# Kernel optimization log

Hardware: AMD Instinct MI355X
Metric: run time of the kernel (lower is better)

## Reference

```python
import jax, jax.numpy as jnp
from jax import lax
import numpy as np

# Model constants (from init_kwargs)
N = 256      # encoder channels
K = 16       # encoder kernel
S = 8        # encoder stride
BOT = 256    # bottleneck dim
NM = 8       # number of BiMamba blocks
DS = 16      # d_state
DC = 4       # d_conv
DI = 512     # d_inner = expand * bot_dim
DTR = 16     # dt_rank = ceil(bot_dim/16)
BATCH = 2
T = 8000


def silu(x):
    return x * jax.nn.sigmoid(x)


def rmsnorm(x, w, eps=1e-5):
    return x * w / jnp.sqrt(jnp.mean(x * x, axis=-1, keepdims=True) + eps)


def selective_scan(xc, dt, Bm, Cm, A, Dp):
    # xc, dt: [B,L,DI]; Bm, Cm: [B,L,DS]; A: [DI,DS]; Dp: [DI]
    Bsz = xc.shape[0]

    def step(h, inp):
        dt_t, B_t, C_t, x_t = inp          # [B,DI],[B,DS],[B,DS],[B,DI]
        dA = jnp.exp(dt_t[:, :, None] * A)  # [B,DI,DS]
        h = dA * h + (dt_t * x_t)[:, :, None] * B_t[:, None, :]
        y = jnp.einsum('bds,bs->bd', h, C_t)
        return h, y

    h0 = jnp.zeros((Bsz, DI, DS), xc.dtype)
    xs = (jnp.swapaxes(dt, 0, 1), jnp.swapaxes(Bm, 0, 1),
          jnp.swapaxes(Cm, 0, 1), jnp.swapaxes(xc, 0, 1))
    _, ys = lax.scan(step, h0, xs)
    return jnp.swapaxes(ys, 0, 1) + xc * Dp


def mamba_dir(x, inw, cw, cb, xpw, dtw, dtb, Alog, Dp, ow):
    # x: [B,L,BOT] -> [B,L,BOT], one Mamba direction
    xz = x @ inw.T                              # [B,L,2*DI]
    xi, z = jnp.split(xz, 2, axis=-1)
    # causal depthwise conv over time
    xc = lax.conv_general_dilated(jnp.swapaxes(xi, 1, 2), cw[:, None, :], (1,),
                                  [(DC - 1, 0)], feature_group_count=DI,
                                  dimension_numbers=('NCH', 'OIH', 'NCH'))
    xc = jnp.swapaxes(silu(xc + cb[None, :, None]), 1, 2)   # [B,L,DI]
    xdbl = xc @ xpw.T                          # [B,L,DTR+2*DS]
    dt = jax.nn.softplus(xdbl[..., :DTR] @ dtw.T + dtb)     # [B,L,DI]
    Bm = xdbl[..., DTR:DTR + DS]
    Cm = xdbl[..., DTR + DS:]
    A = -jnp.exp(Alog)                          # [DI,DS]
    y = selective_scan(xc, dt, Bm, Cm, A, Dp)
    return (y * silu(z)) @ ow.T


def _forward(mixture, enc_w, dec_w, gn_w, gn_b, bot_w, bot_b, blk_norm_w,
             in_w, conv_w, conv_b, xproj_w, dt_w, dt_b, A_log, Dmat, out_w,
             normf_w, mask_w, mask_b):
    # Encoder: Conv1d(1,N,K,stride=S) + ReLU -> mixture_w [B,N,L]
    mw = lax.conv_general_dilated(mixture[:, None, :], enc_w, (S,), 'VALID',
                                  dimension_numbers=('NCH', 'OIH', 'NCH'))
    mw = jax.nn.relu(mw)
    # GroupNorm(1, N): normalize over (C,L) per sample
    mu = jnp.mean(mw, axis=(1, 2), keepdims=True)
    var = jnp.var(mw, axis=(1, 2), keepdims=True)
    x = (mw - mu) / jnp.sqrt(var + 1e-5) * gn_w[None, :, None] + gn_b[None, :, None]
    # 1x1 bottleneck conv -> [B,L,BOT]
    x = jnp.einsum('on,bnl->bol', bot_w, x) + bot_b[None, :, None]
    x = jnp.swapaxes(x, 1, 2)
    # BiMamba blocks: pre-RMSNorm, fwd + reversed Mamba, residual
    for i in range(NM):
        xn = rmsnorm(x, blk_norm_w[i])
        yf = mamba_dir(xn, in_w[i, 0], conv_w[i, 0], conv_b[i, 0], xproj_w[i, 0],
                       dt_w[i, 0], dt_b[i, 0], A_log[i, 0], Dmat[i, 0], out_w[i, 0])
        yb = jnp.flip(mamba_dir(jnp.flip(xn, 1), in_w[i, 1], conv_w[i, 1],
                                conv_b[i, 1], xproj_w[i, 1], dt_w[i, 1],
                                dt_b[i, 1], A_log[i, 1], Dmat[i, 1], out_w[i, 1]), 1)
        x = x + yf + yb
    x = rmsnorm(x, normf_w)
    x = jnp.swapaxes(x, 1, 2)                  # [B,BOT,L]
    # mask head: 1x1 conv -> [B, C*N=N, L], ReLU mask (C=1)
    masks = jnp.einsum('ob,bbl->obl'.replace('bbl', 'xbl').replace('obl', 'xol'), mask_w, x)  # placeholder
    masks = jnp.einsum('ob,xbl->xol', mask_w, x) + mask_b[None, :, None]
    masks = jax.nn.relu(masks)
    masked = mw * masks                        # [B,N,L]
    # Decoder: ConvTranspose1d(N,1,K,stride=S,bias=False)
    wt = jnp.swapaxes(jnp.flip(dec_w, -1), 0, 1)   # [1,N,K]
    y = lax.conv_general_dilated(masked, wt, (1,), [(K - 1, K - 1)],
                                 lhs_dilation=(S,),
                                 dimension_numbers=('NCH', 'OIH', 'NCH'))
    return y[:, 0, :]                          # [B,T], C=1 squeezed


def setup_inputs() -> dict:
    key = jax.random.key(0)
    ks = jax.random.split(key, 12)

    def nrm(k, shape, s=0.05):
        return jax.random.normal(k, shape, jnp.float32) * s

    inp = {
        'mixture': jax.random.normal(ks[0], (BATCH, T), jnp.float32),
        'enc_w': nrm(ks[1], (N, 1, K), 0.1),
        'dec_w': nrm(ks[2], (N, 1, K), 0.1),
        'gn_w': jnp.ones((N,), jnp.float32),
        'gn_b': jnp.zeros((N,), jnp.float32),
        'bot_w': nrm(ks[3], (BOT, N)),
        'bot_b': jnp.zeros((BOT,), jnp.float32),
        'blk_norm_w': jnp.ones((NM, BOT), jnp.float32),
        'in_w': nrm(ks[4], (NM, 2, 2 * DI, BOT)),
        'conv_w': nrm(ks[5], (NM, 2, DI, DC), 0.2),
        'conv_b': jnp.zeros((NM, 2, DI), jnp.float32),
        'xproj_w': nrm(ks[6], (NM, 2, DTR + 2 * DS, DI)),
        'dt_w': nrm(ks[7], (NM, 2, DI, DTR), 0.1),
        'dt_b': jnp.full((NM, 2, DI), -4.0, jnp.float32),
        'A_log': jnp.log(jnp.arange(1., DS + 1, dtype=jnp.float32)) * jnp.ones((NM, 2, DI, DS), jnp.float32),
        'Dmat': jnp.ones((NM, 2, DI), jnp.float32),
        'out_w': nrm(ks[8], (NM, 2, BOT, DI)),
        'normf_w': jnp.ones((BOT,), jnp.float32),
        'mask_w': nrm(ks[9], (N, BOT)),
        'mask_b': jnp.zeros((N,), jnp.float32),
    }
    return inp


def reference(mixture, enc_w, dec_w, gn_w, gn_b, bot_w, bot_b, blk_norm_w,
              in_w, conv_w, conv_b, xproj_w, dt_w, dt_b, A_log, Dmat, out_w,
              normf_w, mask_w, mask_b):
    return _forward(mixture, enc_w, dec_w, gn_w, gn_b, bot_w, bot_b,
                    blk_norm_w, in_w, conv_w, conv_b, xproj_w, dt_w, dt_b,
                    A_log, Dmat, out_w, normf_w, mask_w, mask_b)
```

## Files before the change

kernel.cpp:

```cpp
#include <hip/hip_runtime.h>
#include <cstdint>
#include <cmath>

#define LQ   999
#define BLQ  1998
#define NCH  256
#define NLTOT 255744
#define NCHK 16
#define CHL  64

typedef __attribute__((ext_vector_type(8))) short bf16x8;
typedef __attribute__((ext_vector_type(4))) float f32x4;

__device__ inline ushort f2bf(float f) {
  uint32_t u = __float_as_uint(f);
  u += 0x7fff + ((u >> 16) & 1);
  return (ushort)(u >> 16);
}

__global__ __launch_bounds__(256) void k_quant(const float* __restrict__ inw,
                                               const float* __restrict__ outw,
                                               const float* __restrict__ dtw,
                                               ushort* __restrict__ inwh,
                                               ushort* __restrict__ outwh,
                                               float* __restrict__ dtwt) {
  int i = blockIdx.x * 256 + threadIdx.x;
  if (i < 4194304) inwh[i] = f2bf(inw[i]);
  if (i < 2097152) outwh[i] = f2bf(outw[i]);
  if (i < 131072) {
    int w = i >> 13, d = (i >> 4) & 511, q = i & 15;
    dtwt[(w << 13) + q * 512 + d] = dtw[i];
  }
}

__global__ __launch_bounds__(256) void k_enc(const float* __restrict__ mix,
                                             const float* __restrict__ ew,
                                             float* __restrict__ mw,
                                             float* __restrict__ stats) {
  int t = threadIdx.x;
  int b = blockIdx.x >= LQ;
  int rem = (blockIdx.x - b * LQ) * 256 + t;
  int n = rem / LQ;
  int l = rem - n * LQ;
  const float* mp = mix + b * 8000 + l * 8;
  const float* wp = ew + n * 16;
  float acc = 0.f;
#pragma unroll
  for (int k = 0; k < 16; ++k) acc += mp[k] * wp[k];
  float v = fmaxf(acc, 0.f);
  mw[(b * NCH + n) * LQ + l] = v;
  float s1 = v, s2 = v * v;
#pragma unroll
  for (int off = 32; off >= 1; off >>= 1) {
    s1 += __shfl_xor(s1, off, 64);
    s2 += __shfl_xor(s2, off, 64);
  }
  __shared__ float r1[4], r2[4];
  int wv = t >> 6, lane = t & 63;
  if (lane == 0) { r1[wv] = s1; r2[wv] = s2; }
  __syncthreads();
  if (t == 0) {
    atomicAdd(&stats[b * 2 + 0], r1[0] + r1[1] + r1[2] + r1[3]);
    atomicAdd(&stats[b * 2 + 1], r2[0] + r2[1] + r2[2] + r2[3]);
  }
}

__global__ void k_stats(float* stats) {
  int t = threadIdx.x;
  if (t < 2) {
    float s = stats[t * 2 + 0], q = stats[t * 2 + 1];
    float mu = s / (float)NLTOT;
    float var = q / (float)NLTOT - mu * mu;
    stats[4 + t * 2 + 0] = mu;
    stats[4 + t * 2 + 1] = 1.f / sqrtf(var + 1e-5f);
  }
}

__global__ __launch_bounds__(256) void k_prep(const float* __restrict__ bw,
                                              const float* __restrict__ gw,
                                              const float* __restrict__ gb,
                                              const float* __restrict__ bb,
                                              const float* __restrict__ stats,
                                              float* __restrict__ w2,
                                              float* __restrict__ cc) {
  int o = blockIdx.x, n = threadIdx.x;
  float bwv = bw[o * 256 + n];
  float w2v = bwv * gw[n];
  w2[o * 256 + n] = w2v;
  float s1 = bwv * gb[n], s2 = w2v;
#pragma unroll
  for (int off = 32; off >= 1; off >>= 1) {
    s1 += __shfl_xor(s1, off, 64);
    s2 += __shfl_xor(s2, off, 64);
  }
  __shared__ float r1[4], r2[4];
  int wv = n >> 6, lane = n & 63;
  if (lane == 0) { r1[wv] = s1; r2[wv] = s2; }
  __syncthreads();
  if (n == 0) {
    float a1 = r1[0] + r1[1] + r1[2] + r1[3];
    float a2 = r2[0] + r2[1] + r2[2] + r2[3];
    for (int b = 0; b < 2; ++b)
      cc[b * 256 + o] = bb[o] + a1 - stats[4 + b * 2] * stats[5 + b * 2] * a2;
  }
}

template <bool BF>
__global__ __launch_bounds__(256) void k_rms(const float* __restrict__ x,
                                             const float* __restrict__ w,
                                             float* __restrict__ out,
                                             ushort* __restrict__ outh) {
  int t = threadIdx.x;
  int row = blockIdx.x * 4 + (t >> 6);
  int lane = t & 63;
  if (row >= BLQ) return;
  float4 v = *(const float4*)&x[row * 256 + lane * 4];
  float ss = v.x * v.x + v.y * v.y + v.z * v.z + v.w * v.w;
#pragma unroll
  for (int off = 32; off >= 1; off >>= 1) ss += __shfl_xor(ss, off, 64);
  float r = 1.f / sqrtf(ss * (1.f / 256.f) + 1e-5f);
  float4 wv = *(const float4*)&w[lane * 4];
  float4 o;
  o.x = v.x * wv.x * r; o.y = v.y * wv.y * r;
  o.z = v.z * wv.z * r; o.w = v.w * wv.w * r;
  if (BF) {
    ushort4 oh = {f2bf(o.x), f2bf(o.y), f2bf(o.z), f2bf(o.w)};
    *(ushort4*)&outh[row * 256 + lane * 4] = oh;
  } else {
    *(float4*)&out[row * 256 + lane * 4] = o;
  }
}

template <int MODE>
__global__ __launch_bounds__(256) void gemm64(const float* __restrict__ A,
                                              const float* __restrict__ Bw,
                                              float* __restrict__ C,
                                              const float* __restrict__ aux1,
                                              const float* __restrict__ aux2,
                                              int M, int K,
                                              int aDS, int bDS, int cDS) {
  if (MODE == 4) {
    A += (size_t)blockIdx.z * aDS;
    Bw += (size_t)blockIdx.z * bDS;
    C += (size_t)blockIdx.z * cDS;
  }
  __shared__ float As[16][68];
  __shared__ float Bs[16][68];
  int t = threadIdx.x;
  int m0 = blockIdx.x * 64, n0 = blockIdx.y * 64;
  int tx = t & 15, ty = t >> 4;
  float acc[4][4] = {};
  for (int kk = 0; kk < K; kk += 16) {
    if (MODE == 0) {
#pragma unroll
      for (int j = 0; j < 4; ++j) {
        int e = t + 256 * j;
        int m_ = e & 63, k_ = e >> 6;
        int m = m0 + m_;
        float v = 0.f;
        if (m < M) {
          int bb = m >= LQ;
          int l = m - bb * LQ;
          v = A[(size_t)((bb << 8) + kk + k_) * LQ + l];
        }
        As[k_][m_] = v;
      }
    } else {
      int m_ = t >> 2, k4 = (t & 3) * 4;
      int m = m0 + m_;
      float4 v = make_float4(0.f, 0.f, 0.f, 0.f);
      if (m < M) v = *(const float4*)&A[(size_t)m * K + kk + k4];
      As[k4 + 0][m_] = v.x; As[k4 + 1][m_] = v.y;
      As[k4 + 2][m_] = v.z; As[k4 + 3][m_] = v.w;
    }
    {
      int n_ = t >> 2, k4 = (t & 3) * 4;
      int n = n0 + n_;
      float4 v = make_float4(0.f, 0.f, 0.f, 0.f);
      if (MODE != 4 || n_ < 48)
        v = *(const float4*)&Bw[(size_t)n * K + kk + k4];
      Bs[k4 + 0][n_] = v.x; Bs[k4 + 1][n_] = v.y;
      Bs[k4 + 2][n_] = v.z; Bs[k4 + 3][n_] = v.w;
    }
    __syncthreads();
#pragma unroll
    for (int k = 0; k < 16; ++k) {
      float4 av = *(const float4*)&As[k][ty * 4];
      float4 bv = *(const float4*)&Bs[k][tx * 4];
      acc[0][0] += av.x * bv.x; acc[0][1] += av.x * bv.y; acc[0][2] += av.x * bv.z; acc[0][3] += av.x * bv.w;
      acc[1][0] += av.y * bv.x; acc[1][1] += av.y * bv.y; acc[1][2] += av.y * bv.z; acc[1][3] += av.y * bv.w;
      acc[2][0] += av.z * bv.x; acc[2][1] += av.z * bv.y; acc[2][2] += av.z * bv.z; acc[2][3] += av.z * bv.w;
      acc[3][0] += av.w * bv.x; acc[3][1] += av.w * bv.y; acc[3][2] += av.w * bv.z; acc[3][3] += av.w * bv.w;
    }
    __syncthreads();
  }
#pragma unroll
  for (int i = 0; i < 4; ++i) {
    int m = m0 + ty * 4 + i;
    if (m < M) {
      int n = n0 + tx * 4;
      if (MODE == 0) {
        int bb = m >= LQ;
        float invb = aux1[5 + bb * 2];
        float4 cv = *(const float4*)&aux2[(bb << 8) + n];
        float4 o;
        o.x = acc[i][0] * invb + cv.x; o.y = acc[i][1] * invb + cv.y;
        o.z = acc[i][2] * invb + cv.z; o.w = acc[i][3] * invb + cv.w;
        *(float4*)&C[(size_t)m * 256 + n] = o;
      } else if (MODE == 3) {
        int bb = m >= LQ;
        int l = m - bb * LQ;
        float4 o;
#pragma unroll
        for (int j = 0; j < 4; ++j) {
          int nc = n + j;
          float v = fmaxf(acc[i][j] + aux1[nc], 0.f);
          float mwv = aux2[(size_t)((bb << 8) + nc) * LQ + l];
          ((float*)&o)[j] = v * mwv;
        }
        *(float4*)&C[(size_t)m * 256 + n] = o;
      } else {
#pragma unroll
        for (int j = 0; j < 4; ++j) {
          int nc = n + j;
          if (nc < 48) C[(size_t)m * 48 + nc] = acc[i][j];
        }
      }
    }
  }
}

__global__ __launch_bounds__(256) void k_mm1(const ushort* __restrict__ Ah,
                                             const ushort* __restrict__ Bh,
                                             float* __restrict__ C) {
  int lane = threadIdx.x & 63, wid = threadIdx.x >> 6;
  int mbase = blockIdx.x * 128 + (wid >> 1) * 64;
  int nbase = blockIdx.y * 128 + (wid & 1) * 64;
  int lm = lane & 15, lk = (lane >> 4) * 8;
  f32x4 acc[4][4] = {};
  for (int ks = 0; ks < 256; ks += 32) {
    bf16x8 a[4], b[4];
#pragma unroll
    for (int mi = 0; mi < 4; ++mi) {
      int row = mbase + mi * 16 + lm;
      row = row < BLQ ? row : BLQ - 1;
      a[mi] = *(const bf16x8*)&Ah[(size_t)row * 256 + ks + lk];
    }
#pragma unroll
    for (int ni = 0; ni < 4; ++ni) {
      int nr = nbase + ni * 16 + lm;
      b[ni] = *(const bf16x8*)&Bh[(size_t)nr * 256 + ks + lk];
    }
#pragma unroll
    for (int mi = 0; mi < 4; ++mi)
#pragma unroll
      for (int ni = 0; ni < 4; ++ni)
        acc[mi][ni] = __builtin_amdgcn_mfma_f32_16x16x32_bf16(a[mi], b[ni], acc[mi][ni], 0, 0, 0);
  }
  int rbase = (lane >> 4) * 4;
#pragma unroll
  for (int mi = 0; mi < 4; ++mi)
#pragma unroll
    for (int r = 0; r < 4; ++r) {
      int m = mbase + mi * 16 + rbase + r;
      if (m < BLQ) {
#pragma unroll
        for (int ni = 0; ni < 4; ++ni)
          C[(size_t)m * 2048 + nbase + ni * 16 + lm] = acc[mi][ni][r];
      }
    }
}

__global__ __launch_bounds__(256) void k_mm2(const ushort* __restrict__ Ah,
                                             const ushort* __restrict__ Bh,
                                             float* __restrict__ C) {
  int lane = threadIdx.x & 63, wid = threadIdx.x >> 6;
  int mbase = blockIdx.x * 128 + (wid >> 1) * 64;
  int nbase = blockIdx.y * 128 + (wid & 1) * 64;
  int lm = lane & 15, lk = (lane >> 4) * 8;
  f32x4 acc[4][4] = {};
  for (int ks = 0; ks < 1024; ks += 32) {
    int dir = ks >> 9;
    int di = (ks & 511) + lk;
    const ushort* Ab = Ah + (size_t)dir * BLQ * 512 + di;
    const ushort* Bb = Bh + (size_t)dir * 131072 + di;
    bf16x8 a[4], b[4];
#pragma unroll
    for (int mi = 0; mi < 4; ++mi) {
      int row = mbase + mi * 16 + lm;
      row = row < BLQ ? row : BLQ - 1;
      a[mi] = *(const bf16x8*)&Ab[(size_t)row * 512];
    }
#pragma unroll
    for (int ni = 0; ni < 4; ++ni) {
      int nr = nbase + ni * 16 + lm;
      b[ni] = *(const bf16x8*)&Bb[(size_t)nr * 512];
    }
#pragma unroll
    for (int mi = 0; mi < 4; ++mi)
#pragma unroll
      for (int ni = 0; ni < 4; ++ni)
        acc[mi][ni] = __builtin_amdgcn_mfma_f32_16x16x32_bf16(a[mi], b[ni], acc[mi][ni], 0, 0, 0);
  }
  int rbase = (lane >> 4) * 4;
#pragma unroll
  for (int mi = 0; mi < 4; ++mi)
#pragma unroll
    for (int r = 0; r < 4; ++r) {
      int m = mbase + mi * 16 + rbase + r;
      if (m < BLQ) {
#pragma unroll
        for (int ni = 0; ni < 4; ++ni) {
          size_t idx = (size_t)m * 256 + nbase + ni * 16 + lm;
          C[idx] += acc[mi][ni][r];
        }
      }
    }
}

__global__ __launch_bounds__(256) void k_conv(const float* __restrict__ xz,
                                              const float* __restrict__ cwAll,
                                              const float* __restrict__ cbAll,
                                              float* __restrict__ xc, int blk) {
  int dir = blockIdx.y;
  int flat = blockIdx.x * 256 + threadIdx.x;
  int d = flat & 511, bl = flat >> 9;
  int bb = bl >= LQ;
  int l = bl - bb * LQ;
  int w = blk * 2 + dir;
  const float* cw = cwAll + (size_t)(w * 512 + d) * 4;
  float acc = cbAll[w * 512 + d];
  int zoff = dir * 1024 + d;
#pragma unroll
  for (int j = 0; j < 4; ++j) {
    int ls = (dir == 0) ? (l - 3 + j) : (l + 3 - j);
    if (ls >= 0 && ls < LQ) acc += xz[(size_t)(bb * LQ + ls) * 2048 + zoff] * cw[j];
  }
  float sg = acc / (1.f + __expf(-acc));
  xc[(size_t)(dir * BLQ + bl) * 512 + d] = sg;
}

__global__ __launch_bounds__(256) void k_dt(const float* __restrict__ xdbl,
                                            const float* __restrict__ dtwt,
                                            const float* __restrict__ dtbAll,
                                            float* __restrict__ dtg, int blk) {
  int dir = blockIdx.y;
  int flat = blockIdx.x * 256 + threadIdx.x;
  int d = flat & 511, bl = flat >> 9;
  int w = blk * 2 + dir;
  const float* xd = xdbl + (size_t)(dir * BLQ + bl) * 48;
  const float* Wp = dtwt + (w << 13);
  float acc = dtbAll[w * 512 + d];
#pragma unroll
  for (int q = 0; q < 16; ++q) acc += xd[q] * Wp[q * 512 + d];
  float sp = fmaxf(acc, 0.f) + log1pf(expf(-fabsf(acc)));
  dtg[(size_t)(dir * BLQ + bl) * 512 + d] = sp;
}

__global__ __launch_bounds__(256) void k_scanA(const float* __restrict__ dtg,
                                               const float* __restrict__ xc,
                                               const float* __restrict__ xdbl,
                                               const float* __restrict__ alog,
                                               float* __restrict__ prod,
                                               float* __restrict__ loc, int blk) {
  __shared__ float s_dx[64 * 17 * 2];
  __shared__ float s_bc[64 * 16 * 2];
  int t = threadIdx.x;
  int bid = blockIdx.x;
  int cpair = bid & 7;
  int wb = bid >> 3;
  int dg = wb & 31;
  int b = (wb >> 5) & 1;
  int dir = wb >> 6;
  int dloc = t >> 4, s = t & 15;
  int d0 = dg * 16;
  int d = d0 + dloc;
  int w = blk * 2 + dir;
  int b999 = b * LQ;
  float a2 = -__expf(alog[(size_t)(w * 512 + d) * 16 + s]) * 1.44269504f;
  const float* dtp = dtg + (size_t)dir * BLQ * 512;
  const float* xcp = xc + (size_t)dir * BLQ * 512;
  const float* xdp = xdbl + (size_t)dir * BLQ * 48;
  size_t wbase = (size_t)wb * 4096;
  int c0 = cpair * 2;

  auto stage = [&](int cc) {
    int j16 = t >> 4, dl = t & 15;
#pragma unroll
    for (int it = 0; it < 4; ++it) {
      int j = it * 16 + j16;
      int tg = cc * 64 + j;
      float dtv = 0.f, xv = 0.f;
      if (tg < LQ) {
        int l = dir ? (LQ - 1 - tg) : tg;
        size_t bl = (size_t)(b999 + l);
        dtv = dtp[bl * 512 + d0 + dl];
        xv = xcp[bl * 512 + d0 + dl];
      }
      s_dx[(j * 17 + dl) * 2] = dtv;
      s_dx[(j * 17 + dl) * 2 + 1] = xv;
    }
    int j8 = t >> 5, idx = t & 31;
#pragma unroll
    for (int it = 0; it < 8; ++it) {
      int j = it * 8 + j8;
      int tg = cc * 64 + j;
      float v = 0.f;
      if (tg < LQ) {
        int l = dir ? (LQ - 1 - tg) : tg;
        v = xdp[(size_t)(b999 + l) * 48 + 16 + idx];
      }
      int ss = idx & 15, isC = idx >> 4;
      s_bc[(j * 16 + ss) * 2 + isC] = v;
    }
  };

#pragma unroll
  for (int ci = 0; ci < 2; ++ci) {
    int cc = c0 + ci;
    stage(cc);
    __syncthreads();
    float h = 0.f, pr = 1.f;
#pragma unroll 16
    for (int j = 0; j < 64; ++j) {
      float2 dx = *(float2*)&s_dx[(j * 17 + dloc) * 2];
      float Bv = s_bc[(j * 16 + s) * 2];
      float dA = exp2f(dx.x * a2);
      pr *= dA;
      h = dA * h + dx.x * dx.y * Bv;
    }
    prod[wbase + cc * 256 + t] = pr;
    loc[wbase + cc * 256 + t] = h;
    __syncthreads();
  }
}

__global__ __launch_bounds__(256) void k_scanC(const float* __restrict__ dtg,
                                               const float* __restrict__ xc,
                                               const float* __restrict__ xdbl,
                                               const float* __restrict__ xz,
                                               const float* __restrict__ alog,
                                               const float* __restrict__ dmat,
                                               const float* __restrict__ prod,
                                               const float* __restrict__ loc,
                                               ushort* __restrict__ gh, int blk) {
  __shared__ float s_dx[64 * 17 * 2];
  __shared__ float s_bc[64 * 16 * 2];
  int t = threadIdx.x;
  int bid = blockIdx.x;
  int cpair = bid & 7;
  int wb = bid >> 3;
  int dg = wb & 31;
  int b = (wb >> 5) & 1;
  int dir = wb >> 6;
  int dloc = t >> 4, s = t & 15;
  int d0 = dg * 16;
  int d = d0 + dloc;
  int w = blk * 2 + dir;
  int b999 = b * LQ;
  float a2 = -__expf(alog[(size_t)(w * 512 + d) * 16 + s]) * 1.44269504f;
  float Dd = dmat[w * 512 + d];
  const float* dtp = dtg + (size_t)dir * BLQ * 512;
  const float* xcp = xc + (size_t)dir * BLQ * 512;
  const float* xdp = xdbl + (size_t)dir * BLQ * 48;
  const float* zp = xz + dir * 1024 + 512 + d;
  ushort* gp = gh + (size_t)dir * BLQ * 512;
  size_t wbase = (size_t)wb * 4096;
  int c0 = cpair * 2;

  auto stage = [&](int cc) {
    int j16 = t >> 4, dl = t & 15;
#pragma unroll
    for (int it = 0; it < 4; ++it) {
      int j = it * 16 + j16;
      int tg = cc * 64 + j;
      float dtv = 0.f, xv = 0.f;
      if (tg < LQ) {
        int l = dir ? (LQ - 1 - tg) : tg;
        size_t bl = (size_t)(b999 + l);
        dtv = dtp[bl * 512 + d0 + dl];
        xv = xcp[bl * 512 + d0 + dl];
      }
      s_dx[(j * 17 + dl) * 2] = dtv;
      s_dx[(j * 17 + dl) * 2 + 1] = xv;
    }
    int j8 = t >> 5, idx = t & 31;
#pragma unroll
    for (int it = 0; it < 8; ++it) {
      int j = it * 8 + j8;
      int tg = cc * 64 + j;
      float v = 0.f;
      if (tg < LQ) {
        int l = dir ? (LQ - 1 - tg) : tg;
        v = xdp[(size_t)(b999 + l) * 48 + 16 + idx];
      }
      int ss = idx & 15, isC = idx >> 4;
      s_bc[(j * 16 + ss) * 2 + isC] = v;
    }
  };

  float hs0 = 0.f, hs1 = 0.f;
  {
    float h = 0.f;
#pragma unroll
    for (int ccc = 0; ccc < NCHK; ++ccc) {
      if (ccc == c0) hs0 = h;
      if (ccc == c0 + 1) hs1 = h;
      float prv = prod[wbase + ccc * 256 + t];
      float lov = loc[wbase + ccc * 256 + t];
      h = prv * h + lov;
    }
  }

  auto zload = [&](int cc, int j0n) -> float {
    int tg = cc * 64 + j0n + s;
    if (j0n < 64 && tg < LQ) {
      int l = dir ? (LQ - 1 - tg) : tg;
      return zp[(size_t)(b999 + l) * 2048];
    }
    return 0.f;
  };

#pragma unroll
  for (int ci = 0; ci < 2; ++ci) {
    int cc = c0 + ci;
    stage(cc);
    __syncthreads();
    float h = ci ? hs1 : hs0;
    float keepP = 0.f;
    float zq = zload(cc, 0);
    for (int j0 = 0; j0 < 64; j0 += 16) {
#pragma unroll
      for (int jj = 0; jj < 16; ++jj) {
        int j = j0 + jj;
        float2 dx = *(float2*)&s_dx[(j * 17 + dloc) * 2];
        float2 bc = *(float2*)&s_bc[(j * 16 + s) * 2];
        float dA = exp2f(dx.x * a2);
        h = dA * h + dx.x * dx.y * bc.x;
        float p = h * bc.y;
        p += __shfl_xor(p, 1, 16);
        p += __shfl_xor(p, 2, 16);
        p += __shfl_xor(p, 4, 16);
        p += __shfl_xor(p, 8, 16);
        if (jj == s) keepP = p;
      }
      int tg = cc * 64 + j0 + s;
      float xv = s_dx[((j0 + s) * 17 + dloc) * 2 + 1];
      float zv = zq;
      zq = zload(cc, j0 + 16);
      float sig = 1.f / (1.f + __expf(-zv));
      float y = (keepP + xv * Dd) * (zv * sig);
      if (tg < LQ) {
        int l = dir ? (LQ - 1 - tg) : tg;
        gp[(size_t)(b999 + l) * 512 + d] = f2bf(y);
      }
    }
    __syncthreads();
  }
}

__global__ __launch_bounds__(256) void k_zg(const float* __restrict__ Mt,
                                            const float* __restrict__ dw,
                                            float* __restrict__ Z) {
  __shared__ float sm[16][260];
  __shared__ float sw[256][16];
  int t = threadIdx.x;
  int b = blockIdx.x >= 63;
  int r0 = (blockIdx.x - b * 63) * 16;
#pragma unroll
  for (int it = 0; it < 16; ++it) {
    int e = it * 256 + t;
    int r = e >> 8, c = e & 255;
    int l = r0 + r;
    sm[r][c] = (l < LQ) ? Mt[(size_t)(b * LQ + l) * 256 + c] : 0.f;
    sw[e >> 4][e & 15] = dw[e];
  }
  __syncthreads();
  int lrow = t >> 4, j = t & 15;
  float acc = 0.f;
#pragma unroll 8
  for (int n = 0; n < 256; ++n) acc += sm[lrow][n] * sw[n][j];
  int l = r0 + lrow;
  Z[(size_t)(b * 1008 + l) * 16 + j] = acc;
}

__global__ __launch_bounds__(256) void k_comb(const float* __restrict__ Z,
                                              float* __restrict__ out) {
  int idx = blockIdx.x * 256 + threadIdx.x;
  if (idx >= 16000) return;
  int b = idx >= 8000;
  int tt = idx - b * 8000;
  int l0 = tt >> 3, j0 = tt & 7;
  float v = 0.f;
  if (l0 <= LQ - 1) v += Z[(size_t)(b * 1008 + l0) * 16 + j0];
  if (l0 >= 1) v += Z[(size_t)(b * 1008 + l0 - 1) * 16 + j0 + 8];
  out[idx] = v;
}

extern "C" void kernel_launch(void* const* d_in, const int* in_sizes, int n_in,
                              void* d_out, int out_size, void* d_ws, size_t ws_size,
                              hipStream_t stream) {
  const float* mixture = (const float*)d_in[0];
  const float* enc_w = (const float*)d_in[1];
  const float* dec_w = (const float*)d_in[2];
  const float* gn_w = (const float*)d_in[3];
  const float* gn_b = (const float*)d_in[4];
  const float* bot_w = (const float*)d_in[5];
  const float* bot_b = (const float*)d_in[6];
  const float* blk_norm_w = (const float*)d_in[7];
  const float* in_w = (const float*)d_in[8];
  const float* conv_w = (const float*)d_in[9];
  const float* conv_b = (const float*)d_in[10];
  const float* xproj_w = (const float*)d_in[11];
  const float* dt_w = (const float*)d_in[12];
  const float* dt_b = (const float*)d_in[13];
  const float* A_log = (const float*)d_in[14];
  const float* Dmat = (const float*)d_in[15];
  const float* out_w = (const float*)d_in[16];
  const float* normf_w = (const float*)d_in[17];
  const float* mask_w = (const float*)d_in[18];
  const float* mask_b = (const float*)d_in[19];
  float* outp = (float*)d_out;

  float* W = (float*)d_ws;
  size_t off = 0;
  auto alloc = [&](size_t n) {
    float* p = W + off;
    off += (n + 255) & ~(size_t)255;
    return p;
  };
  float* stats = alloc(8);
  float* w2 = alloc(65536);
  float* cc = alloc(512);
  float* mw = alloc(511488);
  float* x = alloc(511488);
  float* xn = alloc(511488);
  float* xzb = alloc(4091904);
  float* xcb = alloc(2045952);
  float* xdblb = alloc(191808);
  float* dtgb = alloc(2045952);
  float* maskedb = alloc(511488);
  float* prodb = alloc(524288);
  float* locb = alloc(524288);
  float* zbuf = alloc(32256);
  float* dtwt = alloc(131072);
  ushort* xnh = (ushort*)alloc(255744);
  ushort* ghb = (ushort*)alloc(1022976);
  ushort* inwh = (ushort*)alloc(2097152);
  ushort* outwh = (ushort*)alloc(1048576);

  k_quant<<<16384, 256, 0, stream>>>(in_w, out_w, dt_w, inwh, outwh, dtwt);
  hipMemsetAsync(stats, 0, 32, stream);
  k_enc<<<1998, 256, 0, stream>>>(mixture, enc_w, mw, stats);
  k_stats<<<1, 64, 0, stream>>>(stats);
  k_prep<<<256, 256, 0, stream>>>(bot_w, gn_w, gn_b, bot_b, stats, w2, cc);
  gemm64<0><<<dim3(32, 4, 1), 256, 0, stream>>>(mw, w2, x, stats, cc, BLQ, 256, 0, 0, 0);

  for (int i = 0; i < 8; ++i) {
    k_rms<true><<<500, 256, 0, stream>>>(x, blk_norm_w + i * 256, nullptr, xnh);
    k_mm1<<<dim3(16, 16), 256, 0, stream>>>(xnh, inwh + (size_t)i * 524288, xzb);
    k_conv<<<dim3(3996, 2, 1), 256, 0, stream>>>(xzb, conv_w, conv_b, xcb, i);
    gemm64<4><<<dim3(32, 1, 2), 256, 0, stream>>>(
        xcb, xproj_w + (size_t)i * 2 * 48 * 512, xdblb, nullptr, nullptr, BLQ, 512,
        BLQ * 512, 48 * 512, BLQ * 48);
    k_dt<<<dim3(3996, 2, 1), 256, 0, stream>>>(xdblb, dtwt, dt_b, dtgb, i);
    k_scanA<<<1024, 256, 0, stream>>>(dtgb, xcb, xdblb, A_log, prodb, locb, i);
    k_scanC<<<1024, 256, 0, stream>>>(dtgb, xcb, xdblb, xzb, A_log, Dmat, prodb, locb, ghb, i);
    k_mm2<<<dim3(16, 2), 256, 0, stream>>>(ghb, outwh + (size_t)i * 262144, x);
  }

  k_rms<false><<<500, 256, 0, stream>>>(x, normf_w, xn, nullptr);
  gemm64<3><<<dim3(32, 4, 1), 256, 0, stream>>>(xn, mask_w, maskedb, mask_b, mw, BLQ, 256, 0, 0, 0);
  k_zg<<<126, 256, 0, stream>>>(maskedb, dec_w, zbuf);
  k_comb<<<63, 256, 0, stream>>>(zbuf, outp);
}
```

Baseline: 1.532 ms.

## Fuse conv into x_proj GEMM, recompute dt in scan, drop stats atomics

The depthwise causal conv plus SiLU now runs inside the x_proj GEMM's A-tile load and writes xc as a side output. The dt projection and softplus are recomputed inside both scan kernels instead of being stored in a dt buffer. This removes two kernel launches per block and a full-size dt write and read. The encoder statistics now use per-block partial sums reduced by a two-block kernel instead of global atomics plus a memset. The cost is that the x_proj grid stays at only 64 blocks while now doing the conv work, and dt is recomputed twice.

```diff
diff --git a/kernel.cpp b/kernel.cpp
--- a/kernel.cpp
+++ b/kernel.cpp
@@ -16,6 +16,10 @@
   uint32_t u = __float_as_uint(f);
   u += 0x7fff + ((u >> 16) & 1);
   return (ushort)(u >> 16);
+}
+
+__device__ inline float softplusf(float x) {
+  return fmaxf(x, 0.f) + log1pf(expf(-fabsf(x)));
 }
 
 __global__ __launch_bounds__(256) void k_quant(const float* __restrict__ inw,
@@ -36,7 +40,7 @@
 __global__ __launch_bounds__(256) void k_enc(const float* __restrict__ mix,
                                              const float* __restrict__ ew,
                                              float* __restrict__ mw,
-                                             float* __restrict__ stats) {
+                                             float* __restrict__ pp) {
   int t = threadIdx.x;
   int b = blockIdx.x >= LQ;
   int rem = (blockIdx.x - b * LQ) * 256 + t;
@@ -60,19 +64,36 @@
   if (lane == 0) { r1[wv] = s1; r2[wv] = s2; }
   __syncthreads();
   if (t == 0) {
-    atomicAdd(&stats[b * 2 + 0], r1[0] + r1[1] + r1[2] + r1[3]);
-    atomicAdd(&stats[b * 2 + 1], r2[0] + r2[1] + r2[2] + r2[3]);
-  }
-}
-
-__global__ void k_stats(float* stats) {
+    pp[blockIdx.x * 2 + 0] = r1[0] + r1[1] + r1[2] + r1[3];
+    pp[blockIdx.x * 2 + 1] = r2[0] + r2[1] + r2[2] + r2[3];
+  }
+}
+
+__global__ __launch_bounds__(256) void k_stats(const float* __restrict__ pp,
+                                               float* __restrict__ stats) {
   int t = threadIdx.x;
-  if (t < 2) {
-    float s = stats[t * 2 + 0], q = stats[t * 2 + 1];
-    float mu = s / (float)NLTOT;
-    float var = q / (float)NLTOT - mu * mu;
-    stats[4 + t * 2 + 0] = mu;
-    stats[4 + t * 2 + 1] = 1.f / sqrtf(var + 1e-5f);
+  int b = blockIdx.x;
+  float s1 = 0.f, s2 = 0.f;
+  for (int i = t; i < LQ; i += 256) {
+    s1 += pp[(b * LQ + i) * 2 + 0];
+    s2 += pp[(b * LQ + i) * 2 + 1];
+  }
+#pragma unroll
+  for (int off = 32; off >= 1; off >>= 1) {
+    s1 += __shfl_xor(s1, off, 64);
+    s2 += __shfl_xor(s2, off, 64);
+  }
+  __shared__ float r1[4], r2[4];
+  int wv = t >> 6, lane = t & 63;
+  if (lane == 0) { r1[wv] = s1; r2[wv] = s2; }
+  __syncthreads();
+  if (t == 0) {
+    float S1 = r1[0] + r1[1] + r1[2] + r1[3];
+    float S2 = r2[0] + r2[1] + r2[2] + r2[3];
+    float mu = S1 / (float)NLTOT;
+    float var = S2 / (float)NLTOT - mu * mu;
+    stats[4 + b * 2] = mu;
+    stats[5 + b * 2] = 1.f / sqrtf(var + 1e-5f);
   }
 }
 
@@ -137,13 +158,7 @@
                                               float* __restrict__ C,
                                               const float* __restrict__ aux1,
                                               const float* __restrict__ aux2,
-                                              int M, int K,
-                                              int aDS, int bDS, int cDS) {
-  if (MODE == 4) {
-    A += (size_t)blockIdx.z * aDS;
-    Bw += (size_t)blockIdx.z * bDS;
-    C += (size_t)blockIdx.z * cDS;
-  }
+                                              int M, int K) {
   __shared__ float As[16][68];
   __shared__ float Bs[16][68];
   int t = threadIdx.x;
@@ -176,9 +191,7 @@
     {
       int n_ = t >> 2, k4 = (t & 3) * 4;
       int n = n0 + n_;
-      float4 v = make_float4(0.f, 0.f, 0.f, 0.f);
-      if (MODE != 4 || n_ < 48)
-        v = *(const float4*)&Bw[(size_t)n * K + kk + k4];
+      float4 v = *(const float4*)&Bw[(size_t)n * K + kk + k4];
       Bs[k4 + 0][n_] = v.x; Bs[k4 + 1][n_] = v.y;
       Bs[k4 + 2][n_] = v.z; Bs[k4 + 3][n_] = v.w;
     }
@@ -207,7 +220,7 @@
         o.x = acc[i][0] * invb + cv.x; o.y = acc[i][1] * invb + cv.y;
         o.z = acc[i][2] * invb + cv.z; o.w = acc[i][3] * invb + cv.w;
         *(float4*)&C[(size_t)m * 256 + n] = o;
-      } else if (MODE == 3) {
+      } else {
         int bb = m >= LQ;
         int l = m - bb * LQ;
         float4 o;
@@ -219,12 +232,6 @@
           ((float*)&o)[j] = v * mwv;
         }
         *(float4*)&C[(size_t)m * 256 + n] = o;
-      } else {
-#pragma unroll
-        for (int j = 0; j < 4; ++j) {
-          int nc = n + j;
-          if (nc < 48) C[(size_t)m * 48 + nc] = acc[i][j];
-        }
       }
     }
   }
@@ -318,48 +325,95 @@
     }
 }
 
-__global__ __launch_bounds__(256) void k_conv(const float* __restrict__ xz,
-                                              const float* __restrict__ cwAll,
-                                              const float* __restrict__ cbAll,
-                                              float* __restrict__ xc, int blk) {
-  int dir = blockIdx.y;
-  int flat = blockIdx.x * 256 + threadIdx.x;
-  int d = flat & 511, bl = flat >> 9;
-  int bb = bl >= LQ;
-  int l = bl - bb * LQ;
+__global__ __launch_bounds__(256) void k_xproj(const float* __restrict__ xz,
+                                               const float* __restrict__ cwAll,
+                                               const float* __restrict__ cbAll,
+                                               const float* __restrict__ Bw,
+                                               float* __restrict__ xc,
+                                               float* __restrict__ xdbl,
+                                               int blk) {
+  int dir = blockIdx.z;
   int w = blk * 2 + dir;
-  const float* cw = cwAll + (size_t)(w * 512 + d) * 4;
-  float acc = cbAll[w * 512 + d];
-  int zoff = dir * 1024 + d;
-#pragma unroll
-  for (int j = 0; j < 4; ++j) {
-    int ls = (dir == 0) ? (l - 3 + j) : (l + 3 - j);
-    if (ls >= 0 && ls < LQ) acc += xz[(size_t)(bb * LQ + ls) * 2048 + zoff] * cw[j];
-  }
-  float sg = acc / (1.f + __expf(-acc));
-  xc[(size_t)(dir * BLQ + bl) * 512 + d] = sg;
-}
-
-__global__ __launch_bounds__(256) void k_dt(const float* __restrict__ xdbl,
-                                            const float* __restrict__ dtwt,
-                                            const float* __restrict__ dtbAll,
-                                            float* __restrict__ dtg, int blk) {
-  int dir = blockIdx.y;
-  int flat = blockIdx.x * 256 + threadIdx.x;
-  int d = flat & 511, bl = flat >> 9;
-  int w = blk * 2 + dir;
-  const float* xd = xdbl + (size_t)(dir * BLQ + bl) * 48;
-  const float* Wp = dtwt + (w << 13);
-  float acc = dtbAll[w * 512 + d];
-#pragma unroll
-  for (int q = 0; q < 16; ++q) acc += xd[q] * Wp[q * 512 + d];
-  float sp = fmaxf(acc, 0.f) + log1pf(expf(-fabsf(acc)));
-  dtg[(size_t)(dir * BLQ + bl) * 512 + d] = sp;
-}
-
-__global__ __launch_bounds__(256) void k_scanA(const float* __restrict__ dtg,
-                                               const float* __restrict__ xc,
+  const float* Bwp = Bw + (size_t)dir * 48 * 512;
+  float* xcp = xc + (size_t)dir * BLQ * 512;
+  float* xdp = xdbl + (size_t)dir * BLQ * 48;
+  __shared__ float As[16][68];
+  __shared__ float Bs[16][68];
+  int t = threadIdx.x;
+  int m0 = blockIdx.x * 64;
+  int tx = t & 15, ty = t >> 4;
+  float acc[4][4] = {};
+  for (int kk = 0; kk < 512; kk += 16) {
+    {
+      int m_ = t >> 2, k4q = (t & 3) * 4;
+      int m = m0 + m_;
+      float4 v = make_float4(0.f, 0.f, 0.f, 0.f);
+      if (m < BLQ) {
+        int bb = m >= LQ;
+        int l = m - bb * LQ;
+        int d = kk + k4q;
+        float4 cw0 = *(const float4*)&cwAll[(size_t)(w * 512 + d + 0) * 4];
+        float4 cw1 = *(const float4*)&cwAll[(size_t)(w * 512 + d + 1) * 4];
+        float4 cw2 = *(const float4*)&cwAll[(size_t)(w * 512 + d + 2) * 4];
+        float4 cw3 = *(const float4*)&cwAll[(size_t)(w * 512 + d + 3) * 4];
+        float4 a = *(const float4*)&cbAll[w * 512 + d];
+#pragma unroll
+        for (int j = 0; j < 4; ++j) {
+          int ls = dir ? (l + 3 - j) : (l - 3 + j);
+          if (ls >= 0 && ls < LQ) {
+            float4 xv = *(const float4*)&xz[(size_t)(bb * LQ + ls) * 2048 + dir * 1024 + d];
+            a.x += xv.x * ((const float*)&cw0)[j];
+            a.y += xv.y * ((const float*)&cw1)[j];
+            a.z += xv.z * ((const float*)&cw2)[j];
+            a.w += xv.w * ((const float*)&cw3)[j];
+          }
+        }
+        v.x = a.x / (1.f + __expf(-a.x));
+        v.y = a.y / (1.f + __expf(-a.y));
+        v.z = a.z / (1.f + __expf(-a.z));
+        v.w = a.w / (1.f + __expf(-a.w));
+        *(float4*)&xcp[(size_t)m * 512 + d] = v;
+      }
+      As[k4q + 0][m_] = v.x; As[k4q + 1][m_] = v.y;
+      As[k4q + 2][m_] = v.z; As[k4q + 3][m_] = v.w;
+    }
+    {
+      int n_ = t >> 2, k4 = (t & 3) * 4;
+      float4 v = make_float4(0.f, 0.f, 0.f, 0.f);
+      if (n_ < 48) v = *(const float4*)&Bwp[(size_t)n_ * 512 + kk + k4];
+      Bs[k4 + 0][n_] = v.x; Bs[k4 + 1][n_] = v.y;
+      Bs[k4 + 2][n_] = v.z; Bs[k4 + 3][n_] = v.w;
+    }
+    __syncthreads();
+#pragma unroll
+    for (int k = 0; k < 16; ++k) {
+      float4 av = *(const float4*)&As[k][ty * 4];
+      float4 bv = *(const float4*)&Bs[k][tx * 4];
+      acc[0][0] += av.x * bv.x; acc[0][1] += av.x * bv.y; acc[0][2] += av.x * bv.z; acc[0][3] += av.x * bv.w;
+      acc[1][0] += av.y * bv.x; acc[1][1] += av.y * bv.y; acc[1][2] += av.y * bv.z; acc[1][3] += av.y * bv.w;
+      acc[2][0] += av.z * bv.x; acc[2][1] += av.z * bv.y; acc[2][2] += av.z * bv.z; acc[2][3] += av.z * bv.w;
+      acc[3][0] += av.w * bv.x; acc[3][1] += av.w * bv.y; acc[3][2] += av.w * bv.z; acc[3][3] += av.w * bv.w;
+    }
+    __syncthreads();
+  }
+#pragma unroll
+  for (int i = 0; i < 4; ++i) {
+    int m = m0 + ty * 4 + i;
+    if (m < BLQ) {
+      int n = tx * 4;
+#pragma unroll
+      for (int j = 0; j < 4; ++j) {
+        int nc = n + j;
+        if (nc < 48) xdp[(size_t)m * 48 + nc] = acc[i][j];
+      }
+    }
+  }
+}
+
+__global__ __launch_bounds__(256) void k_scanA(const float* __restrict__ xc,
                                                const float* __restrict__ xdbl,
+                                               const float* __restrict__ dtwt,
+                                               const float* __restrict__ dtb,
                                                const float* __restrict__ alog,
                                                float* __restrict__ prod,
                                                float* __restrict__ loc, int blk) {
@@ -378,9 +432,10 @@
   int w = blk * 2 + dir;
   int b999 = b * LQ;
   float a2 = -__expf(alog[(size_t)(w * 512 + d) * 16 + s]) * 1.44269504f;
-  const float* dtp = dtg + (size_t)dir * BLQ * 512;
   const float* xcp = xc + (size_t)dir * BLQ * 512;
   const float* xdp = xdbl + (size_t)dir * BLQ * 48;
+  const float* Wt = dtwt + (w << 13);
+  float dtbv_ = dtb[w * 512 + d0 + (t & 15)];
   size_t wbase = (size_t)wb * 4096;
   int c0 = cpair * 2;
 
@@ -394,8 +449,12 @@
       if (tg < LQ) {
         int l = dir ? (LQ - 1 - tg) : tg;
         size_t bl = (size_t)(b999 + l);
-        dtv = dtp[bl * 512 + d0 + dl];
         xv = xcp[bl * 512 + d0 + dl];
+        const float* xd = xdp + bl * 48;
+        float acc = dtbv_;
+#pragma unroll
+        for (int q = 0; q < 16; ++q) acc += xd[q] * Wt[q * 512 + d0 + dl];
+        dtv = softplusf(acc);
       }
       s_dx[(j * 17 + dl) * 2] = dtv;
       s_dx[(j * 17 + dl) * 2 + 1] = xv;
@@ -435,9 +494,10 @@
   }
 }
 
-__global__ __launch_bounds__(256) void k_scanC(const float* __restrict__ dtg,
-                                               const float* __restrict__ xc,
+__global__ __launch_bounds__(256) void k_scanC(const float* __restrict__ xc,
                                                const float* __restrict__ xdbl,
+                                               const float* __restrict__ dtwt,
+                                               const float* __restrict__ dtb,
                                                const float* __restrict__ xz,
                                                const float* __restrict__ alog,
                                                const float* __restrict__ dmat,
@@ -460,9 +520,10 @@
   int b999 = b * LQ;
   float a2 = -__expf(alog[(size_t)(w * 512 + d) * 16 + s]) * 1.44269504f;
   float Dd = dmat[w * 512 + d];
-  const float* dtp = dtg + (size_t)dir * BLQ * 512;
   const float* xcp = xc + (size_t)dir * BLQ * 512;
   const float* xdp = xdbl + (size_t)dir * BLQ * 48;
+  const float* Wt = dtwt + (w << 13);
+  float dtbv_ = dtb[w * 512 + d0 + (t & 15)];
   const float* zp = xz + dir * 1024 + 512 + d;
   ushort* gp = gh + (size_t)dir * BLQ * 512;
   size_t wbase = (size_t)wb * 4096;
@@ -478,8 +539,12 @@
       if (tg < LQ) {
         int l = dir ? (LQ - 1 - tg) : tg;
         size_t bl = (size_t)(b999 + l);
-        dtv = dtp[bl * 512 + d0 + dl];
         xv = xcp[bl * 512 + d0 + dl];
+        const float* xd = xdp + bl * 48;
+        float acc = dtbv_;
+#pragma unroll
+        for (int q = 0; q < 16; ++q) acc += xd[q] * Wt[q * 512 + d0 + dl];
+        dtv = softplusf(acc);
       }
       s_dx[(j * 17 + dl) * 2] = dtv;
       s_dx[(j * 17 + dl) * 2 + 1] = xv;
@@ -630,6 +695,7 @@
     return p;
   };
   float* stats = alloc(8);
+  float* pp = alloc(4096);
   float* w2 = alloc(65536);
   float* cc = alloc(512);
   float* mw = alloc(511488);
@@ -638,7 +704,6 @@
   float* xzb = alloc(4091904);
   float* xcb = alloc(2045952);
   float* xdblb = alloc(191808);
-  float* dtgb = alloc(2045952);
   float* maskedb = alloc(511488);
   float* prodb = alloc(524288);
   float* locb = alloc(524288);
@@ -650,27 +715,24 @@
   ushort* outwh = (ushort*)alloc(1048576);
 
   k_quant<<<16384, 256, 0, stream>>>(in_w, out_w, dt_w, inwh, outwh, dtwt);
-  hipMemsetAsync(stats, 0, 32, stream);
-  k_enc<<<1998, 256, 0, stream>>>(mixture, enc_w, mw, stats);
-  k_stats<<<1, 64, 0, stream>>>(stats);
+  k_enc<<<1998, 256, 0, stream>>>(mixture, enc_w, mw, pp);
+  k_stats<<<2, 256, 0, stream>>>(pp, stats);
   k_prep<<<256, 256, 0, stream>>>(bot_w, gn_w, gn_b, bot_b, stats, w2, cc);
-  gemm64<0><<<dim3(32, 4, 1), 256, 0, stream>>>(mw, w2, x, stats, cc, BLQ, 256, 0, 0, 0);
+  gemm64<0><<<dim3(32, 4, 1), 256, 0, stream>>>(mw, w2, x, stats, cc, BLQ, 256);
 
   for (int i = 0; i < 8; ++i) {
     k_rms<true><<<500, 256, 0, stream>>>(x, blk_norm_w + i * 256, nullptr, xnh);
     k_mm1<<<dim3(16, 16), 256, 0, stream>>>(xnh, inwh + (size_t)i * 524288, xzb);
-    k_conv<<<dim3(3996, 2, 1), 256, 0, stream>>>(xzb, conv_w, conv_b, xcb, i);
-    gemm64<4><<<dim3(32, 1, 2), 256, 0, stream>>>(
-        xcb, xproj_w + (size_t)i * 2 * 48 * 512, xdblb, nullptr, nullptr, BLQ, 512,
-        BLQ * 512, 48 * 512, BLQ * 48);
-    k_dt<<<dim3(3996, 2, 1), 256, 0, stream>>>(xdblb, dtwt, dt_b, dtgb, i);
-    k_scanA<<<1024, 256, 0, stream>>>(dtgb, xcb, xdblb, A_log, prodb, locb, i);
-    k_scanC<<<1024, 256, 0, stream>>>(dtgb, xcb, xdblb, xzb, A_log, Dmat, prodb, locb, ghb, i);
+    k_xproj<<<dim3(32, 1, 2), 256, 0, stream>>>(
+        xzb, conv_w, conv_b, xproj_w + (size_t)i * 2 * 48 * 512, xcb, xdblb, i);
+    k_scanA<<<1024, 256, 0, stream>>>(xcb, xdblb, dtwt, dt_b, A_log, prodb, locb, i);
+    k_scanC<<<1024, 256, 0, stream>>>(xcb, xdblb, dtwt, dt_b, xzb, A_log, Dmat,
+                                      prodb, locb, ghb, i);
     k_mm2<<<dim3(16, 2), 256, 0, stream>>>(ghb, outwh + (size_t)i * 262144, x);
   }
 
   k_rms<false><<<500, 256, 0, stream>>>(x, normf_w, xn, nullptr);
-  gemm64<3><<<dim3(32, 4, 1), 256, 0, stream>>>(xn, mask_w, maskedb, mask_b, mw, BLQ, 256, 0, 0, 0);
+  gemm64<3><<<dim3(32, 4, 1), 256, 0, stream>>>(xn, mask_w, maskedb, mask_b, mw, BLQ, 256);
   k_zg<<<126, 256, 0, stream>>>(maskedb, dec_w, zbuf);
   k_comb<<<63, 256, 0, stream>>>(zbuf, outp);
 }
```

After: 1.790 ms. 16.8% more time.
